# Kernel tuning notes

Measured on AMD Instinct MI355X. Metric: run time of the kernel, lower is better.

## Reference

```python
import math
import jax, jax.numpy as jnp
import numpy as np

H, N2, B, L = 256, 32, 8, 4096
DT_MIN, DT_MAX = 1e-3, 1e-1

def setup_inputs() -> dict:
    key = jax.random.key(0)
    ks = jax.random.split(key, 6)
    u = jax.random.normal(ks[0], (B, H, L), dtype=jnp.float32)
    # log_dt uniform in [log(dt_min), log(dt_max)] as in S4DKernel.__init__
    log_dt = jax.random.uniform(ks[1], (H,), dtype=jnp.float32) * (
        math.log(DT_MAX) - math.log(DT_MIN)) + math.log(DT_MIN)
    C = jax.random.normal(ks[2], (H, N2, 2), dtype=jnp.float32)  # view_as_real of complex C
    log_A_real = jnp.log(0.5 * jnp.ones((H, N2), dtype=jnp.float32))
    A_imag = math.pi * jnp.broadcast_to(jnp.arange(N2, dtype=jnp.float32), (H, N2))
    D = jax.random.normal(ks[3], (H,), dtype=jnp.float32)
    W = jax.random.normal(ks[4], (2 * H, H), dtype=jnp.float32) / math.sqrt(H)
    b = jax.random.normal(ks[5], (2 * H,), dtype=jnp.float32) * 0.01
    return {"u": u, "log_dt": log_dt, "C": C, "log_A_real": log_A_real,
            "A_imag": A_imag, "D": D, "W": W, "b": b}

def reference(u, log_dt, C, log_A_real, A_imag, D, W, b):
    # ---- S4DKernel: generate convolution kernel k (H, L) ----
    Lk = u.shape[-1]
    dt = jnp.exp(log_dt)                                  # (H,)
    Cc = C[..., 0] + 1j * C[..., 1]                       # (H, N2) complex
    A = -jnp.exp(log_A_real) + 1j * A_imag                # (H, N2) complex
    dtA = A * dt[:, None]                                 # (H, N2)
    # Vandermonde: exp(dtA * l) for l in [0, L)  -> (H, N2, L) complex
    K = jnp.exp(dtA[:, :, None] * jnp.arange(Lk, dtype=jnp.float32))
    Ct = Cc * (jnp.exp(dtA) - 1.0) / A                    # (H, N2)
    k = 2.0 * jnp.einsum('hn,hnl->hl', Ct, K).real        # (H, L) float32
    # ---- FFT long convolution ----
    n = 2 * Lk
    k_f = jnp.fft.rfft(k, n=n)                            # (H, n//2+1)
    u_f = jnp.fft.rfft(u, n=n)                            # (B, H, n//2+1)
    y = jnp.fft.irfft(u_f * k_f, n=n)[..., :Lk]           # (B, H, L)
    y = y + u * D[:, None]                                # skip connection
    y = jax.nn.gelu(y, approximate=False)                 # nn.GELU (exact)
    # ---- output 1x1 conv (H -> 2H) + GLU over channel dim ----
    z = jnp.einsum('oh,bhl->bol', W, y) + b[None, :, None]  # (B, 2H, L)
    a, g = jnp.split(z, 2, axis=1)
    return a * jax.nn.sigmoid(g)                          # (B, H, L)
```

## Files before the change

### kernel.cpp

```cpp
#include <hip/hip_runtime.h>
#include <math.h>

#define H 256
#define N2 32
#define Bsz 8
#define Lseq 4096
#define BH (Bsz*H)
#define NCH 32
#define LC (Lseq/NCH)
#define HN (H*N2)

#define S_OFF  0
#define Y_OFF  (S_OFF + BH*NCH*N2*2)
#define WB_OFF (Y_OFF + (BH*Lseq/2))
#define TB_OFF (WB_OFF + (512*256/2))
#define EB_OFF (TB_OFF + (H*128*128/2))
#define VB_OFF (EB_OFF + (H*128*64/2))

typedef __attribute__((ext_vector_type(8))) short bf16x8;
typedef __attribute__((ext_vector_type(8))) unsigned short u16x8;
typedef __attribute__((ext_vector_type(4))) float f32x4;

__device__ __forceinline__ unsigned short f2bf(float x) {
  union { float f; unsigned int u; } v; v.f = x;
  unsigned int r = v.u + 0x7fffu + ((v.u >> 16) & 1u);
  return (unsigned short)(r >> 16);
}
__device__ __forceinline__ unsigned int packbf(float lo, float hi) {
  return (unsigned int)f2bf(lo) | ((unsigned int)f2bf(hi) << 16);
}
__device__ __forceinline__ float bf2f(unsigned short b) {
  union { unsigned int u; float f; } v; v.u = ((unsigned int)b) << 16;
  return v.f;
}

__global__ __launch_bounds__(128) void k_prep(const float* __restrict__ log_dt,
                                              const float* __restrict__ C,
                                              const float* __restrict__ lar,
                                              const float* __restrict__ aim,
                                              const float* __restrict__ W,
                                              unsigned short* __restrict__ Wb,
                                              unsigned short* __restrict__ Tb,
                                              unsigned short* __restrict__ Eb,
                                              unsigned short* __restrict__ Vb) {
  __shared__ unsigned short kbuf[128];
  int h = blockIdx.x;
  int j = threadIdx.x;
  {
    int i = h * 128 + j;
    float4 v = *(const float4*)&W[i * 4];
    uint2 p; p.x = packbf(v.x, v.y); p.y = packbf(v.z, v.w);
    *(uint2*)&Wb[i * 4] = p;
  }
  float dt = expf(log_dt[h]);
  float kacc = 0.f;
  unsigned short* Erow = Eb + (h * 128 + j) * 64;
  for (int n = 0; n < 32; n++) {
    int hn = (h << 5) + n;
    float Ar = -expf(lar[hn]), Ai = aim[hn];
    float dAr = Ar * dt, dAi = Ai * dt;
    float er = expf(dAr), sw, cw;
    sincosf(dAi, &sw, &cw);
    float wr = er * cw, wi = er * sw;
    float emr = wr - 1.f, emi = wi;
    float inv = 1.f / (Ar * Ar + Ai * Ai);
    float qr = (emr * Ar + emi * Ai) * inv;
    float qi = (emi * Ar - emr * Ai) * inv;
    float Cr = C[2 * hn], Ci = C[2 * hn + 1];
    float c2r = 2.f * (Cr * qr - Ci * qi);
    float c2i = 2.f * (Cr * qi + Ci * qr);
    float ej = expf(dAr * (float)j), sj, cj;
    sincosf(dAi * (float)j, &sj, &cj);
    kacc = fmaf(c2r, ej * cj, fmaf(-c2i, ej * sj, kacc));
    float e1 = expf(dAr * (float)(j + 1)), s1, c1;
    sincosf(dAi * (float)(j + 1), &s1, &c1);
    float w1r = e1 * c1, w1i = e1 * s1;
    Erow[2 * n]     = f2bf(c2r * w1r - c2i * w1i);
    Erow[2 * n + 1] = f2bf(-(c2r * w1i + c2i * w1r));
    float ev = expf(dAr * (float)(127 - j)), sv, cv;
    sincosf(dAi * (float)(127 - j), &sv, &cv);
    Vb[(h * 64 + 2 * n) * 128 + j]     = f2bf(ev * cv);
    Vb[(h * 64 + 2 * n + 1) * 128 + j] = f2bf(ev * sv);
  }
  kbuf[j] = f2bf(kacc);
  __syncthreads();
  unsigned short* Trow = Tb + (h * 128 + j) * 128;
#pragma unroll
  for (int s8 = 0; s8 < 16; s8++) {
    u16x8 v;
#pragma unroll
    for (int t = 0; t < 8; t++) {
      int m = s8 * 8 + t;
      v[t] = (j >= m) ? kbuf[j - m] : (unsigned short)0;
    }
    *(u16x8*)&Trow[s8 * 8] = v;
  }
}

__global__ __launch_bounds__(256) void k_state(const float* __restrict__ u,
                                               const unsigned short* __restrict__ Vb,
                                               float* __restrict__ S) {
  __shared__ unsigned short Ul[64][136];
  __shared__ unsigned short Bl[64][136];
  int h   = blockIdx.x;
  int mq  = blockIdx.y;
  int tid = threadIdx.x;
  int wv = tid >> 6, lane = tid & 63;
  int n16 = lane & 15, quad = lane >> 4;
  int m0 = wv * 16;
  f32x4 acc[4] = {};
#pragma unroll
  for (int i = 0; i < 8; i++) {
    int e = tid + i * 256;
    int r = e >> 5, c4 = e & 31;
    int b = mq * 2 + (r >> 5), c = r & 31;
    float4 v = *(const float4*)&u[((b * 256 + h) * 4096 + c * 128 + c4 * 4)];
    *(unsigned int*)&Ul[r][c4 * 4]     = packbf(v.x, v.y);
    *(unsigned int*)&Ul[r][c4 * 4 + 2] = packbf(v.z, v.w);
  }
#pragma unroll
  for (int i = 0; i < 4; i++) {
    int e = tid + i * 256;
    int p = e >> 4, s8 = e & 15;
    *(u16x8*)&Bl[p][s8 * 8] = *(const u16x8*)&Vb[(h * 64 + p) * 128 + s8 * 8];
  }
  __syncthreads();
#pragma unroll
  for (int ks = 0; ks < 128; ks += 32) {
    int kc = ks + quad * 8;
    bf16x8 af = *(const bf16x8*)&Ul[m0 + n16][kc];
#pragma unroll
    for (int nt = 0; nt < 4; nt++) {
      bf16x8 bf = *(const bf16x8*)&Bl[nt * 16 + n16][kc];
      acc[nt] = __builtin_amdgcn_mfma_f32_16x16x32_bf16(af, bf, acc[nt], 0, 0, 0);
    }
  }
#pragma unroll
  for (int reg = 0; reg < 4; reg++) {
    int m = m0 + quad * 4 + reg;
    int b = mq * 2 + (m >> 5), c = m & 31;
#pragma unroll
    for (int nt = 0; nt < 4; nt++) {
      int p = nt * 16 + n16;
      S[((b * 256 + h) * 32 + c) * 64 + p] = acc[nt][reg];
    }
  }
}

__global__ void k_prefix(const float* __restrict__ log_dt, const float* __restrict__ lar,
                         const float* __restrict__ aim, float* __restrict__ S) {
  int t = blockIdx.x * blockDim.x + threadIdx.x;
  if (t >= BH * N2) return;
  int n = t & 31, bh = t >> 5;
  int h = bh & (H - 1);
  int hn = (h << 5) + n;
  float dt  = expf(log_dt[h]);
  float dAr = -expf(lar[hn]) * dt, dAi = aim[hn] * dt;
  float eL = expf(dAr * (float)LC), sL, cL;
  sincosf(dAi * (float)LC, &sL, &cL);
  float wLr = eL * cL, wLi = eL * sL;
  float fr = 0.f, fi = 0.f;
  for (int c = 0; c < NCH; c++) {
    int si = (((bh * NCH + c) << 5) + n) << 1;
    float sr = S[si], s1 = S[si + 1];
    S[si] = fr; S[si + 1] = fi;
    float nr = fmaf(wLr, fr, fmaf(-wLi, fi, sr));
    float ni = fmaf(wLr, fi, fmaf(wLi, fr, s1));
    fr = nr; fi = ni;
  }
}

__global__ __launch_bounds__(256) void k_emit(const float* __restrict__ u,
                                              const float* __restrict__ S,
                                              const unsigned short* __restrict__ Tb,
                                              const unsigned short* __restrict__ Eb,
                                              const float* __restrict__ Dp,
                                              unsigned short* __restrict__ yb) {
  __shared__ unsigned short Ul[64][200];
  __shared__ unsigned short Bl[128][200];
  int h   = blockIdx.x;
  int mq  = blockIdx.y;
  int tid = threadIdx.x;
  int wv = tid >> 6, lane = tid & 63;
  int n16 = lane & 15, quad = lane >> 4;
  int m0 = wv * 16;
  f32x4 acc[8] = {};

#pragma unroll
  for (int i = 0; i < 8; i++) {
    int e = tid + i * 256;
    int r = e >> 5, c4 = e & 31;
    int b = mq * 2 + (r >> 5), c = r & 31;
    float4 v = *(const float4*)&u[((b * 256 + h) * 4096 + c * 128 + c4 * 4)];
    *(unsigned int*)&Ul[r][c4 * 4]     = packbf(v.x, v.y);
    *(unsigned int*)&Ul[r][c4 * 4 + 2] = packbf(v.z, v.w);
  }
#pragma unroll
  for (int i = 0; i < 4; i++) {
    int e = tid + i * 256;
    int r = e >> 4, c4 = e & 15;
    int b = mq * 2 + (r >> 5), c = r & 31;
    float4 v = *(const float4*)&S[((b * 256 + h) * 32 + c) * 64 + c4 * 4];
    *(unsigned int*)&Ul[r][128 + c4 * 4]     = packbf(v.x, v.y);
    *(unsigned int*)&Ul[r][128 + c4 * 4 + 2] = packbf(v.z, v.w);
  }
#pragma unroll
  for (int i = 0; i < 8; i++) {
    int e = tid + i * 256;
    int jj = e >> 4, s8 = e & 15;
    *(u16x8*)&Bl[jj][s8 * 8] = *(const u16x8*)&Tb[(h * 128 + jj) * 128 + s8 * 8];
  }
#pragma unroll
  for (int i = 0; i < 4; i++) {
    int e = tid + i * 256;
    int jj = e >> 3, p8 = e & 7;
    *(u16x8*)&Bl[jj][128 + p8 * 8] = *(const u16x8*)&Eb[(h * 128 + jj) * 64 + p8 * 8];
  }
  __syncthreads();
#pragma unroll
  for (int ks = 0; ks < 192; ks += 32) {
    int kc = ks + quad * 8;
    bf16x8 af = *(const bf16x8*)&Ul[m0 + n16][kc];
#pragma unroll
    for (int nt = 0; nt < 8; nt++) {
      bf16x8 bf = *(const bf16x8*)&Bl[nt * 16 + n16][kc];
      acc[nt] = __builtin_amdgcn_mfma_f32_16x16x32_bf16(af, bf, acc[nt], 0, 0, 0);
    }
  }
  float Dh = Dp[h];
#pragma unroll
  for (int reg = 0; reg < 4; reg++) {
    int m = m0 + quad * 4 + reg;
    int b = mq * 2 + (m >> 5), c = m & 31;
    int base = (b * 256 + h) * 4096 + c * 128;
#pragma unroll
    for (int nt = 0; nt < 8; nt++) {
      int j = nt * 16 + n16;
      float uv = bf2f(Ul[m][j]);
      float v  = fmaf(Dh, uv, acc[nt][reg]);
      float ge = 0.5f * v * (1.0f + erff(v * 0.70710678118654752f));
      yb[base + j] = f2bf(ge);
    }
  }
}

__global__ __launch_bounds__(256) void k_gemm(const unsigned short* __restrict__ yb,
                                              const unsigned short* __restrict__ Wb,
                                              const float* __restrict__ bias,
                                              float* __restrict__ out) {
  __shared__ unsigned short Ws[128][72];
  __shared__ unsigned short Ys[128][72];
  int tid  = threadIdx.x;
  int l0   = blockIdx.x * 128;
  int o0   = blockIdx.y * 64;
  int bb   = blockIdx.z;
  int wave = tid >> 6;
  int lane = tid & 63;
  int wo   = wave & 1;
  int wl   = wave >> 1;
  int n    = lane & 15;
  int quad = lane >> 4;

  f32x4 acc_a[2][4] = {};
  f32x4 acc_g[2][4] = {};

  for (int kk = 0; kk < H; kk += 64) {
#pragma unroll
    for (int i = 0; i < 4; i++) {
      int e = tid + i * 256;
      int r = e >> 3, s = e & 7;
      int gr = (r < 64) ? (o0 + r) : (192 + o0 + r);
      *(u16x8*)&Ws[r][s * 8] = *(const u16x8*)&Wb[gr * 256 + kk + s * 8];
    }
    {
      int kcol = tid & 63;
      int lg0  = tid >> 6;
      const unsigned short* yrow = yb + (bb * 256 + kk + kcol) * 4096 + l0;
#pragma unroll
      for (int i = 0; i < 4; i++) {
        int l8 = (lg0 * 4 + i) * 8;
        u16x8 v = *(const u16x8*)&yrow[l8];
#pragma unroll
        for (int jj = 0; jj < 8; jj++)
          Ys[l8 + jj][kcol] = v[jj];
      }
    }
    __syncthreads();
#pragma unroll
    for (int ks = 0; ks < 64; ks += 32) {
      int kc = ks + quad * 8;
      bf16x8 af_a[2], af_g[2], bfr[4];
#pragma unroll
      for (int mt = 0; mt < 2; mt++) {
        af_a[mt] = *(const bf16x8*)&Ws[wo * 32 + mt * 16 + n][kc];
        af_g[mt] = *(const bf16x8*)&Ws[64 + wo * 32 + mt * 16 + n][kc];
      }
#pragma unroll
      for (int lt = 0; lt < 4; lt++)
        bfr[lt] = *(const bf16x8*)&Ys[wl * 64 + lt * 16 + n][kc];
#pragma unroll
      for (int mt = 0; mt < 2; mt++)
#pragma unroll
        for (int lt = 0; lt < 4; lt++) {
          acc_a[mt][lt] = __builtin_amdgcn_mfma_f32_16x16x32_bf16(af_a[mt], bfr[lt], acc_a[mt][lt], 0, 0, 0);
          acc_g[mt][lt] = __builtin_amdgcn_mfma_f32_16x16x32_bf16(af_g[mt], bfr[lt], acc_g[mt][lt], 0, 0, 0);
        }
    }
    __syncthreads();
  }
#pragma unroll
  for (int mt = 0; mt < 2; mt++) {
    int ob = o0 + wo * 32 + mt * 16 + quad * 4;
#pragma unroll
    for (int reg = 0; reg < 4; reg++) {
      int op = ob + reg;
      float ba = bias[op], bg = bias[H + op];
      float* orow = &out[(bb * H + op) * Lseq + l0 + wl * 64 + n];
#pragma unroll
      for (int lt = 0; lt < 4; lt++) {
        float a = acc_a[mt][lt][reg] + ba;
        float g = acc_g[mt][lt][reg] + bg;
        orow[lt * 16] = a / (1.0f + expf(-g));
      }
    }
  }
}

extern "C" void kernel_launch(void* const* d_in, const int* in_sizes, int n_in,
                              void* d_out, int out_size, void* d_ws, size_t ws_size,
                              hipStream_t stream) {
  const float* u      = (const float*)d_in[0];
  const float* log_dt = (const float*)d_in[1];
  const float* C      = (const float*)d_in[2];
  const float* lar    = (const float*)d_in[3];
  const float* aim    = (const float*)d_in[4];
  const float* Dp     = (const float*)d_in[5];
  const float* W      = (const float*)d_in[6];
  const float* bias   = (const float*)d_in[7];
  float* out = (float*)d_out;
  float* ws  = (float*)d_ws;
  float* S   = ws + S_OFF;
  unsigned short* yb  = (unsigned short*)(ws + Y_OFF);
  unsigned short* Wb  = (unsigned short*)(ws + WB_OFF);
  unsigned short* Tbg = (unsigned short*)(ws + TB_OFF);
  unsigned short* Ebg = (unsigned short*)(ws + EB_OFF);
  unsigned short* Vbg = (unsigned short*)(ws + VB_OFF);

  hipLaunchKernelGGL(k_prep,   dim3(H), dim3(128), 0, stream, log_dt, C, lar, aim, W, Wb, Tbg, Ebg, Vbg);
  hipLaunchKernelGGL(k_state,  dim3(H, 4), dim3(256), 0, stream, u, Vbg, S);
  hipLaunchKernelGGL(k_prefix, dim3(BH * N2 / 256), dim3(256), 0, stream, log_dt, lar, aim, S);
  hipLaunchKernelGGL(k_emit,   dim3(H, 4), dim3(256), 0, stream, u, S, Tbg, Ebg, Dp, yb);
  hipLaunchKernelGGL(k_gemm,   dim3(Lseq / 128, H / 64, Bsz), dim3(256), 0, stream, yb, Wb, bias, out);
}
```

Before: 178.5 us.

## Fuse chunk-state, prefix scan and emit kernels into one per-(b,h) kernel

Merges k_state, k_prefix and k_emit into one kernel, k_ssm, with one block per (batch, head). Chunk states are computed with MFMA into shared memory, scanned across chunks by 32 lanes, and fed directly into the emit GEMM. This removes the global round trip of the state buffer S and two kernel launches. In exchange, the serial 32-step scan runs inside each block while the other waves sit idle, and the Tb/Eb/Vb operands are read directly from global memory instead of being staged in LDS.

```diff
diff --git a/kernel.cpp b/kernel.cpp
--- a/kernel.cpp
+++ b/kernel.cpp
@@ -10,8 +10,7 @@
 #define LC (Lseq/NCH)
 #define HN (H*N2)
 
-#define S_OFF  0
-#define Y_OFF  (S_OFF + BH*NCH*N2*2)
+#define Y_OFF  0
 #define WB_OFF (Y_OFF + (BH*Lseq/2))
 #define TB_OFF (WB_OFF + (512*256/2))
 #define EB_OFF (TB_OFF + (H*128*128/2))
@@ -97,149 +96,111 @@
   }
 }
 
-__global__ __launch_bounds__(256) void k_state(const float* __restrict__ u,
-                                               const unsigned short* __restrict__ Vb,
-                                               float* __restrict__ S) {
-  __shared__ unsigned short Ul[64][136];
-  __shared__ unsigned short Bl[64][136];
-  int h   = blockIdx.x;
-  int mq  = blockIdx.y;
+__global__ __launch_bounds__(256) void k_ssm(const float* __restrict__ u,
+                                             const float* __restrict__ log_dt,
+                                             const float* __restrict__ lar,
+                                             const float* __restrict__ aim,
+                                             const unsigned short* __restrict__ Vb,
+                                             const unsigned short* __restrict__ Tb,
+                                             const unsigned short* __restrict__ Eb,
+                                             const float* __restrict__ Dp,
+                                             unsigned short* __restrict__ yb) {
+  __shared__ unsigned short Ub[32][136];
+  __shared__ float          Fb[32][68];
+  __shared__ unsigned short Fl[32][72];
+  int g   = blockIdx.x;
+  int b   = g & 7, h = g >> 3;
   int tid = threadIdx.x;
   int wv = tid >> 6, lane = tid & 63;
   int n16 = lane & 15, quad = lane >> 4;
-  int m0 = wv * 16;
-  f32x4 acc[4] = {};
-#pragma unroll
-  for (int i = 0; i < 8; i++) {
-    int e = tid + i * 256;
-    int r = e >> 5, c4 = e & 31;
-    int b = mq * 2 + (r >> 5), c = r & 31;
-    float4 v = *(const float4*)&u[((b * 256 + h) * 4096 + c * 128 + c4 * 4)];
-    *(unsigned int*)&Ul[r][c4 * 4]     = packbf(v.x, v.y);
-    *(unsigned int*)&Ul[r][c4 * 4 + 2] = packbf(v.z, v.w);
-  }
-#pragma unroll
-  for (int i = 0; i < 4; i++) {
-    int e = tid + i * 256;
-    int p = e >> 4, s8 = e & 15;
-    *(u16x8*)&Bl[p][s8 * 8] = *(const u16x8*)&Vb[(h * 64 + p) * 128 + s8 * 8];
+  const float* ubase = u + (b * 256 + h) * 4096;
+
+#pragma unroll
+  for (int i = 0; i < 2; i++) {
+    int idx = tid * 2 + i;
+    float4 va = *(const float4*)(ubase + idx * 8);
+    float4 vb4 = *(const float4*)(ubase + idx * 8 + 4);
+    unsigned short* dst = &Ub[idx >> 4][(idx & 15) * 8];
+    *(unsigned int*)(dst)     = packbf(va.x, va.y);
+    *(unsigned int*)(dst + 2) = packbf(va.z, va.w);
+    *(unsigned int*)(dst + 4) = packbf(vb4.x, vb4.y);
+    *(unsigned int*)(dst + 6) = packbf(vb4.z, vb4.w);
   }
   __syncthreads();
-#pragma unroll
-  for (int ks = 0; ks < 128; ks += 32) {
-    int kc = ks + quad * 8;
-    bf16x8 af = *(const bf16x8*)&Ul[m0 + n16][kc];
-#pragma unroll
-    for (int nt = 0; nt < 4; nt++) {
-      bf16x8 bf = *(const bf16x8*)&Bl[nt * 16 + n16][kc];
-      acc[nt] = __builtin_amdgcn_mfma_f32_16x16x32_bf16(af, bf, acc[nt], 0, 0, 0);
-    }
-  }
-#pragma unroll
-  for (int reg = 0; reg < 4; reg++) {
-    int m = m0 + quad * 4 + reg;
-    int b = mq * 2 + (m >> 5), c = m & 31;
-#pragma unroll
-    for (int nt = 0; nt < 4; nt++) {
-      int p = nt * 16 + n16;
-      S[((b * 256 + h) * 32 + c) * 64 + p] = acc[nt][reg];
-    }
-  }
-}
-
-__global__ void k_prefix(const float* __restrict__ log_dt, const float* __restrict__ lar,
-                         const float* __restrict__ aim, float* __restrict__ S) {
-  int t = blockIdx.x * blockDim.x + threadIdx.x;
-  if (t >= BH * N2) return;
-  int n = t & 31, bh = t >> 5;
-  int h = bh & (H - 1);
-  int hn = (h << 5) + n;
-  float dt  = expf(log_dt[h]);
-  float dAr = -expf(lar[hn]) * dt, dAi = aim[hn] * dt;
-  float eL = expf(dAr * (float)LC), sL, cL;
-  sincosf(dAi * (float)LC, &sL, &cL);
-  float wLr = eL * cL, wLi = eL * sL;
-  float fr = 0.f, fi = 0.f;
-  for (int c = 0; c < NCH; c++) {
-    int si = (((bh * NCH + c) << 5) + n) << 1;
-    float sr = S[si], s1 = S[si + 1];
-    S[si] = fr; S[si + 1] = fi;
-    float nr = fmaf(wLr, fr, fmaf(-wLi, fi, sr));
-    float ni = fmaf(wLr, fi, fmaf(wLi, fr, s1));
-    fr = nr; fi = ni;
-  }
-}
-
-__global__ __launch_bounds__(256) void k_emit(const float* __restrict__ u,
-                                              const float* __restrict__ S,
-                                              const unsigned short* __restrict__ Tb,
-                                              const unsigned short* __restrict__ Eb,
-                                              const float* __restrict__ Dp,
-                                              unsigned short* __restrict__ yb) {
-  __shared__ unsigned short Ul[64][200];
-  __shared__ unsigned short Bl[128][200];
-  int h   = blockIdx.x;
-  int mq  = blockIdx.y;
-  int tid = threadIdx.x;
-  int wv = tid >> 6, lane = tid & 63;
-  int n16 = lane & 15, quad = lane >> 4;
-  int m0 = wv * 16;
-  f32x4 acc[8] = {};
-
-#pragma unroll
-  for (int i = 0; i < 8; i++) {
-    int e = tid + i * 256;
-    int r = e >> 5, c4 = e & 31;
-    int b = mq * 2 + (r >> 5), c = r & 31;
-    float4 v = *(const float4*)&u[((b * 256 + h) * 4096 + c * 128 + c4 * 4)];
-    *(unsigned int*)&Ul[r][c4 * 4]     = packbf(v.x, v.y);
-    *(unsigned int*)&Ul[r][c4 * 4 + 2] = packbf(v.z, v.w);
-  }
-#pragma unroll
-  for (int i = 0; i < 4; i++) {
-    int e = tid + i * 256;
-    int r = e >> 4, c4 = e & 15;
-    int b = mq * 2 + (r >> 5), c = r & 31;
-    float4 v = *(const float4*)&S[((b * 256 + h) * 32 + c) * 64 + c4 * 4];
-    *(unsigned int*)&Ul[r][128 + c4 * 4]     = packbf(v.x, v.y);
-    *(unsigned int*)&Ul[r][128 + c4 * 4 + 2] = packbf(v.z, v.w);
-  }
-#pragma unroll
-  for (int i = 0; i < 8; i++) {
-    int e = tid + i * 256;
-    int jj = e >> 4, s8 = e & 15;
-    *(u16x8*)&Bl[jj][s8 * 8] = *(const u16x8*)&Tb[(h * 128 + jj) * 128 + s8 * 8];
-  }
-#pragma unroll
-  for (int i = 0; i < 4; i++) {
-    int e = tid + i * 256;
-    int jj = e >> 3, p8 = e & 7;
-    *(u16x8*)&Bl[jj][128 + p8 * 8] = *(const u16x8*)&Eb[(h * 128 + jj) * 64 + p8 * 8];
+
+  {
+    f32x4 sacc[2] = {};
+#pragma unroll
+    for (int ks = 0; ks < 128; ks += 32) {
+      int kc = ks + quad * 8;
+      bf16x8 bv = *(const bf16x8*)&Vb[(h * 64 + wv * 16 + n16) * 128 + kc];
+#pragma unroll
+      for (int mt = 0; mt < 2; mt++) {
+        bf16x8 av = *(const bf16x8*)&Ub[mt * 16 + n16][kc];
+        sacc[mt] = __builtin_amdgcn_mfma_f32_16x16x32_bf16(av, bv, sacc[mt], 0, 0, 0);
+      }
+    }
+#pragma unroll
+    for (int mt = 0; mt < 2; mt++)
+#pragma unroll
+      for (int reg = 0; reg < 4; reg++)
+        Fb[mt * 16 + quad * 4 + reg][wv * 16 + n16] = sacc[mt][reg];
   }
   __syncthreads();
+
+  if (wv == 0 && lane < 32) {
+    int n = lane, hn = (h << 5) + n;
+    float dt  = expf(log_dt[h]);
+    float dAr = -expf(lar[hn]) * dt, dAi = aim[hn] * dt;
+    float eL = expf(dAr * (float)LC), sL, cL;
+    sincosf(dAi * (float)LC, &sL, &cL);
+    float wLr = eL * cL, wLi = eL * sL;
+    float fr = 0.f, fi = 0.f;
+    for (int c = 0; c < NCH; c++) {
+      float sr = Fb[c][2 * n], si = Fb[c][2 * n + 1];
+      *(unsigned int*)&Fl[c][2 * n] = packbf(fr, fi);
+      float nr = fmaf(wLr, fr, fmaf(-wLi, fi, sr));
+      float ni = fmaf(wLr, fi, fmaf(wLi, fr, si));
+      fr = nr; fi = ni;
+    }
+  }
+  __syncthreads();
+
+  f32x4 acc[2][2] = {};
 #pragma unroll
   for (int ks = 0; ks < 192; ks += 32) {
     int kc = ks + quad * 8;
-    bf16x8 af = *(const bf16x8*)&Ul[m0 + n16][kc];
-#pragma unroll
-    for (int nt = 0; nt < 8; nt++) {
-      bf16x8 bf = *(const bf16x8*)&Bl[nt * 16 + n16][kc];
-      acc[nt] = __builtin_amdgcn_mfma_f32_16x16x32_bf16(af, bf, acc[nt], 0, 0, 0);
-    }
-  }
+    bf16x8 av[2];
+#pragma unroll
+    for (int mt = 0; mt < 2; mt++)
+      av[mt] = (ks < 128) ? *(const bf16x8*)&Ub[mt * 16 + n16][kc]
+                          : *(const bf16x8*)&Fl[mt * 16 + n16][kc - 128];
+#pragma unroll
+    for (int ntl = 0; ntl < 2; ntl++) {
+      int j = (wv * 2 + ntl) * 16 + n16;
+      bf16x8 bv = (ks < 128) ? *(const bf16x8*)&Tb[(h * 128 + j) * 128 + kc]
+                             : *(const bf16x8*)&Eb[(h * 128 + j) * 64 + kc - 128];
+#pragma unroll
+      for (int mt = 0; mt < 2; mt++)
+        acc[mt][ntl] = __builtin_amdgcn_mfma_f32_16x16x32_bf16(av[mt], bv, acc[mt][ntl], 0, 0, 0);
+    }
+  }
+
   float Dh = Dp[h];
-#pragma unroll
-  for (int reg = 0; reg < 4; reg++) {
-    int m = m0 + quad * 4 + reg;
-    int b = mq * 2 + (m >> 5), c = m & 31;
-    int base = (b * 256 + h) * 4096 + c * 128;
-#pragma unroll
-    for (int nt = 0; nt < 8; nt++) {
-      int j = nt * 16 + n16;
-      float uv = bf2f(Ul[m][j]);
-      float v  = fmaf(Dh, uv, acc[nt][reg]);
-      float ge = 0.5f * v * (1.0f + erff(v * 0.70710678118654752f));
-      yb[base + j] = f2bf(ge);
+  unsigned short* ybase = yb + (b * 256 + h) * 4096;
+#pragma unroll
+  for (int mt = 0; mt < 2; mt++) {
+#pragma unroll
+    for (int reg = 0; reg < 4; reg++) {
+      int c = mt * 16 + quad * 4 + reg;
+#pragma unroll
+      for (int ntl = 0; ntl < 2; ntl++) {
+        int j = (wv * 2 + ntl) * 16 + n16;
+        float uv = bf2f(Ub[c][j]);
+        float v  = fmaf(Dh, uv, acc[mt][ntl][reg]);
+        float ge = 0.5f * v * (1.0f + erff(v * 0.70710678118654752f));
+        ybase[c * 128 + j] = f2bf(ge);
+      }
     }
   }
 }
@@ -339,16 +300,13 @@
   const float* bias   = (const float*)d_in[7];
   float* out = (float*)d_out;
   float* ws  = (float*)d_ws;
-  float* S   = ws + S_OFF;
   unsigned short* yb  = (unsigned short*)(ws + Y_OFF);
   unsigned short* Wb  = (unsigned short*)(ws + WB_OFF);
   unsigned short* Tbg = (unsigned short*)(ws + TB_OFF);
   unsigned short* Ebg = (unsigned short*)(ws + EB_OFF);
   unsigned short* Vbg = (unsigned short*)(ws + VB_OFF);
 
-  hipLaunchKernelGGL(k_prep,   dim3(H), dim3(128), 0, stream, log_dt, C, lar, aim, W, Wb, Tbg, Ebg, Vbg);
-  hipLaunchKernelGGL(k_state,  dim3(H, 4), dim3(256), 0, stream, u, Vbg, S);
-  hipLaunchKernelGGL(k_prefix, dim3(BH * N2 / 256), dim3(256), 0, stream, log_dt, lar, aim, S);
-  hipLaunchKernelGGL(k_emit,   dim3(H, 4), dim3(256), 0, stream, u, S, Tbg, Ebg, Dp, yb);
-  hipLaunchKernelGGL(k_gemm,   dim3(Lseq / 128, H / 64, Bsz), dim3(256), 0, stream, yb, Wb, bias, out);
-}
+  hipLaunchKernelGGL(k_prep, dim3(H), dim3(128), 0, stream, log_dt, C, lar, aim, W, Wb, Tbg, Ebg, Vbg);
+  hipLaunchKernelGGL(k_ssm,  dim3(BH), dim3(256), 0, stream, u, log_dt, lar, aim, Vbg, Tbg, Ebg, Dp, yb);
+  hipLaunchKernelGGL(k_gemm, dim3(Lseq / 128, H / 64, Bsz), dim3(256), 0, stream, yb, Wb, bias, out);
+}
```

Measured after the change: 167.3 us. 1.07x faster.
